# Kernel tuning notes

Hardware: AMD Instinct MI355X
Metric: run time of the kernel (lower is better)

The kernel has to match this reference:

```python
import jax, jax.numpy as jnp
import numpy as np

HIDDEN = 512

def setup_inputs() -> dict:
    key = jax.random.key(0)
    ks = jax.random.split(key, 8)
    S, Bsz, I, H, D = 512, 64, 512, HIDDEN, 2
    return {
        "X": jax.random.normal(ks[0], (S, Bsz, I), jnp.float32),
        "W": jax.random.normal(ks[1], (D, 4 * H, I), jnp.float32) * 0.05,
        "R": jax.random.normal(ks[2], (D, 4 * H, H), jnp.float32) * 0.05,
        "B": jax.random.normal(ks[3], (D, 8 * H), jnp.float32) * 0.05,
        "sequence_lens": jax.random.randint(ks[4], (Bsz,), 0, S, jnp.int32),
        "initial_h": jax.random.normal(ks[5], (D, Bsz, H), jnp.float32) * 0.1,
        "initial_c": jax.random.normal(ks[6], (D, Bsz, H), jnp.float32) * 0.1,
        "P": jax.random.normal(ks[7], (D, 3 * H), jnp.float32) * 0.05,
    }

def _run_dir(Xg, R_d, Rb_d, h0, c0, P_d, seq_lens, ts, H):
    # Gate layout along 4H axis: i, o, f, c (ONNX order used by the source).
    P_i, P_f, P_o = P_d[:H], P_d[H:2 * H], P_d[2 * H:3 * H]

    def step(carry, inp):
        h, c = carry
        xg, t = inp                              # xg: [B,4H] precomputed X@W^T + Wb
        g = xg + h @ R_d.T + Rb_d                # [B,4H]
        i_t = jax.nn.sigmoid(g[:, :H] + P_i * c)
        f_t = jax.nn.sigmoid(g[:, 2 * H:3 * H] + P_f * c)
        c_til = jnp.tanh(g[:, 3 * H:4 * H])
        c_new = f_t * c + i_t * c_til
        o_t = jax.nn.sigmoid(g[:, H:2 * H] + P_o * c_new)
        h_new = o_t * jnp.tanh(c_new)
        mask = (t < seq_lens).astype(h_new.dtype)[:, None]
        h_new = h_new * mask + h0 * (1 - mask)
        c_new = c_new * mask + c0 * (1 - mask)
        return (h_new, c_new), h_new

    (h_f, c_f), hs = jax.lax.scan(step, (h0, c0), (Xg[ts], jnp.asarray(ts)))
    return hs, h_f, c_f

def reference(X, W, R, B, sequence_lens, initial_h, initial_c, P):
    S, Bsz, I = X.shape
    D = W.shape[0]
    H = W.shape[1] // 4
    Wb = B[:, :4 * H]
    Rb = B[:, 4 * H:8 * H]
    # Batch the input projection over all timesteps once: [D,S,B,4H]
    Xg_all = jnp.einsum('sbi,dgi->dsbg', X, W) + Wb[:, None, None, :]
    Ys, Yhs, Ycs = [], [], []
    for d in range(D):
        ts = np.arange(S) if d == 0 else np.arange(S)[::-1].copy()
        hs, h_f, c_f = _run_dir(Xg_all[d], R[d], Rb[d], initial_h[d],
                                initial_c[d], P[d], sequence_lens, ts, H)
        if d == 1:
            hs = hs[::-1]                         # scan emitted reversed time order
        Ys.append(hs)
        Yhs.append(h_f)
        Ycs.append(c_f)
    Y = jnp.stack(Ys, axis=1)                     # [S, D, B, H]
    Y_h = jnp.stack(Yhs, axis=0)                  # [D, B, H]
    Y_c = jnp.stack(Ycs, axis=0)                  # [D, B, H]
    return Y, Y_h, Y_c
```

## Files before the change

### kernel.cpp

```cpp
#include <hip/hip_runtime.h>
#include <stdint.h>
#include <stddef.h>

#define S_LEN 512
#define BATCH 64
#define ISZ   512
#define HID   512
#define NDIR  2

typedef short bf16x8 __attribute__((ext_vector_type(8)));
typedef unsigned short u16x8 __attribute__((ext_vector_type(8)));
typedef float f32x4 __attribute__((ext_vector_type(4)));

#define XB_ELEMS  ((size_t)S_LEN * 4 * 8192)
#define HH_ELEMS  ((size_t)NDIR * 513 * 4 * 8192)
#define CNT_BYTES ((size_t)16416)
#define XB_BYTES  (XB_ELEMS * 2)
#define HH_BYTES  (HH_ELEMS * 2)

__device__ __forceinline__ unsigned short f2bf(float f) {
    unsigned int u = __float_as_uint(f);
    u += 0x7fffu + ((u >> 16) & 1u);
    return (unsigned short)(u >> 16);
}

__device__ __forceinline__ int l2_load_i32(const int* p) {
    int v;
    asm volatile("global_load_dword %0, %1, off sc0\n\t"
                 "s_waitcnt vmcnt(0)"
                 : "=v"(v) : "v"(p) : "memory");
    return v;
}

__global__ void k_convX(const float* __restrict__ X, unsigned short* __restrict__ Xb) {
    int gu = blockIdx.x * 256 + threadIdx.x;
    int t   = gu >> 12;
    int rem = gu & 4095;
    int b   = rem >> 6;
    int u   = rem & 63;
    const float* src = X + ((size_t)(t * 64 + b)) * 512 + u * 8;
    float4 a = *(const float4*)(src);
    float4 c = *(const float4*)(src + 4);
    u16x8 o;
    o[0]=f2bf(a.x); o[1]=f2bf(a.y); o[2]=f2bf(a.z); o[3]=f2bf(a.w);
    o[4]=f2bf(c.x); o[5]=f2bf(c.y); o[6]=f2bf(c.z); o[7]=f2bf(c.w);
    int i = b >> 4, br = b & 15;
    size_t off = ((size_t)(t * 4 + i)) * 8192 + (size_t)br * 512 + (size_t)((u ^ (b & 7)) << 3);
    *(u16x8*)(Xb + off) = o;
}

__global__ void k_initH(const float* __restrict__ h0, unsigned short* __restrict__ hh) {
    int gu = blockIdx.x * 256 + threadIdx.x;
    int d   = gu >> 12;
    int rem = gu & 4095;
    int b   = rem >> 6;
    int u   = rem & 63;
    const float* src = h0 + ((size_t)(d * 64 + b)) * 512 + u * 8;
    float4 a = *(const float4*)(src);
    float4 c = *(const float4*)(src + 4);
    u16x8 o;
    o[0]=f2bf(a.x); o[1]=f2bf(a.y); o[2]=f2bf(a.z); o[3]=f2bf(a.w);
    o[4]=f2bf(c.x); o[5]=f2bf(c.y); o[6]=f2bf(c.z); o[7]=f2bf(c.w);
    int i = b >> 4, br = b & 15;
    size_t blk = ((size_t)d * 513 + 0) * 4 + i;
    size_t off = blk * 8192 + (size_t)br * 512 + (size_t)((u ^ (b & 7)) << 3);
    *(u16x8*)(hh + off) = o;
}

__launch_bounds__(256, 1)
__global__ void k_lstm(const float* __restrict__ W, const float* __restrict__ R,
                       const float* __restrict__ Bb, const int* __restrict__ slen,
                       const float* __restrict__ h0g, const float* __restrict__ c0g,
                       const float* __restrict__ P,
                       const unsigned short* __restrict__ Xb,
                       unsigned short* __restrict__ hh,
                       int* __restrict__ cnt,
                       float* __restrict__ Y) {
    __shared__ __align__(16) float gbuf[4 * 256];
    __shared__ int s_xcd[256];
    __shared__ unsigned char s_inv[256];
    __shared__ int s_role, s_fast;

    const int tid = threadIdx.x;
    const int bx  = blockIdx.x;

    int* const arrive = cnt;
    int* const xcdtab = cnt + 288;

    if (tid == 0) {
        int x;
        asm volatile("s_getreg_b32 %0, hwreg(HW_REG_XCC_ID)" : "=s"(x));
        x &= 0xf;
        __hip_atomic_store(&xcdtab[bx], x + 1, __ATOMIC_RELAXED, __HIP_MEMORY_SCOPE_AGENT);
        asm volatile("s_waitcnt vmcnt(0)" ::: "memory");
        __hip_atomic_fetch_add(arrive, 1, __ATOMIC_RELAXED, __HIP_MEMORY_SCOPE_AGENT);
        int iters = 0;
        while (__hip_atomic_load(arrive, __ATOMIC_RELAXED, __HIP_MEMORY_SCOPE_AGENT) < 256) {
            __builtin_amdgcn_s_sleep(1);
            if (++iters > 2000000) break;
        }
    }
    __syncthreads();
    s_xcd[tid] = __hip_atomic_load(&xcdtab[tid], __ATOMIC_RELAXED, __HIP_MEMORY_SCOPE_AGENT) - 1;
    __syncthreads();
    {
        const int myx = s_xcd[tid];
        int r = 0;
        for (int b = 0; b < 256; ++b) {
            const int xb = s_xcd[b];
            r += (int)((xb < myx) | ((xb == myx) & (b < tid)));
        }
        s_inv[r] = (unsigned char)(myx & 0xff);
        if (tid == bx) s_role = r;
    }
    __syncthreads();
    if (tid == 0) {
        const int g0 = s_role & ~31;
        int uni = 1;
        for (int q = 1; q < 32; ++q) uni &= (int)(s_inv[g0 + q] == s_inv[g0]);
        int distinct = 1;
        for (int q = 1; q < 256; ++q) distinct += (int)(s_inv[q] != s_inv[q - 1]);
        s_fast = uni & (int)(distinct >= 2);
    }
    __syncthreads();
    const int  role = s_role;
    const bool fast = (s_fast != 0);
    const int  d = role >> 7;
    const int  i = (role >> 5) & 3;
    const int  j = role & 31;
    int* const gcnt = cnt + 32 + ((role >> 5) << 5);

    const int w  = tid >> 6;
    const int l  = tid & 63;
    const int lr = l & 15;
    const int lq = l >> 4;

    bf16x8 Wf[16], Rf[16];
    {
        const int row = w * 512 + j * 16 + lr;
        const float* wp = W + ((size_t)(d * 2048 + row)) * 512;
        const float* rp = R + ((size_t)(d * 2048 + row)) * 512;
#pragma unroll
        for (int kc = 0; kc < 16; ++kc) {
            int k0 = kc * 32 + lq * 8;
            float4 a = *(const float4*)(wp + k0);
            float4 b4 = *(const float4*)(wp + k0 + 4);
            bf16x8 f;
            f[0]=(short)f2bf(a.x);  f[1]=(short)f2bf(a.y);  f[2]=(short)f2bf(a.z);  f[3]=(short)f2bf(a.w);
            f[4]=(short)f2bf(b4.x); f[5]=(short)f2bf(b4.y); f[6]=(short)f2bf(b4.z); f[7]=(short)f2bf(b4.w);
            Wf[kc] = f;
            a  = *(const float4*)(rp + k0);
            b4 = *(const float4*)(rp + k0 + 4);
            bf16x8 g;
            g[0]=(short)f2bf(a.x);  g[1]=(short)f2bf(a.y);  g[2]=(short)f2bf(a.z);  g[3]=(short)f2bf(a.w);
            g[4]=(short)f2bf(b4.x); g[5]=(short)f2bf(b4.y); g[6]=(short)f2bf(b4.z); g[7]=(short)f2bf(b4.w);
            Rf[kc] = g;
        }
    }

    const int eb = tid >> 4;
    const int ec = tid & 15;
    const int bg = i * 16 + eb;
    const int kh = j * 16 + ec;
    const float bias_i = Bb[d * 4096 + 0 * 512 + kh] + Bb[d * 4096 + 2048 + 0 * 512 + kh];
    const float bias_o = Bb[d * 4096 + 1 * 512 + kh] + Bb[d * 4096 + 2048 + 1 * 512 + kh];
    const float bias_f = Bb[d * 4096 + 2 * 512 + kh] + Bb[d * 4096 + 2048 + 2 * 512 + kh];
    const float bias_c = Bb[d * 4096 + 3 * 512 + kh] + Bb[d * 4096 + 2048 + 3 * 512 + kh];
    const float Pi = P[d * 1536 + kh];
    const float Pf = P[d * 1536 + 512 + kh];
    const float Po = P[d * 1536 + 1024 + kh];
    const int   sl  = slen[bg];
    const float h0v = h0g[((size_t)d * 64 + bg) * 512 + kh];
    const float c0v = c0g[((size_t)d * 64 + bg) * 512 + kh];
    float c_state = c0v;

    const int rbase = lr * 512;
    const int swz   = lr & 7;

    const int peb = tid >> 4;
    const int cp  = (tid & 15) >> 1;
    const size_t puo = (size_t)peb * 256
                     + (size_t)((((2 * j + (cp >> 2)) ^ (peb & 7)) << 2) + (cp & 3));

    for (int ts = 0; ts < 512; ++ts) {
        const int t = (d == 0) ? ts : (511 - ts);

        f32x4 acc = {0.f, 0.f, 0.f, 0.f};
        {
            const unsigned short* xsrc = Xb + ((size_t)(t * 4 + i)) * 8192;
#pragma unroll
            for (int kc = 0; kc < 16; ++kc) {
                int u = (kc * 4 + lq) ^ swz;
                bf16x8 a = *(const bf16x8*)(xsrc + rbase + u * 8);
                acc = __builtin_amdgcn_mfma_f32_16x16x32_bf16(a, Wf[kc], acc, 0, 0, 0);
            }
        }

        if (ts > 0) {
            if (tid == 0) {
                const int target = 32 * ts;
                int iters = 0;
                if (fast) {
                    while (l2_load_i32(gcnt) < target) {
                        __builtin_amdgcn_s_sleep(1);
                        if (++iters > 4000000) break;
                    }
                } else {
                    while (__hip_atomic_load(gcnt, __ATOMIC_RELAXED,
                                             __HIP_MEMORY_SCOPE_AGENT) < target) {
                        __builtin_amdgcn_s_sleep(1);
                        if (++iters > 4000000) break;
                    }
                }
            }
            __syncthreads();
        }

        {
            const unsigned short* hsrc16 = hh + (((size_t)d * 513 + ts) * 4 + i) * 8192;
            if (fast) {
                bf16x8 hf[16];
#pragma unroll
                for (int kc = 0; kc < 16; ++kc) {
                    const int u = (kc * 4 + lq) ^ swz;
                    hf[kc] = *(const bf16x8*)(hsrc16 + rbase + u * 8);
                }
#pragma unroll
                for (int kc = 0; kc < 16; ++kc)
                    acc = __builtin_amdgcn_mfma_f32_16x16x32_bf16(hf[kc], Rf[kc], acc, 0, 0, 0);
            } else {
                const unsigned int* hsrc = (const unsigned int*)hsrc16;
                unsigned int hv[64];
#pragma unroll
                for (int kc = 0; kc < 16; ++kc) {
                    int u = (kc * 4 + lq) ^ swz;
                    const unsigned int* p = hsrc + (lr * 256 + u * 4);
                    hv[kc * 4 + 0] = __hip_atomic_load(p + 0, __ATOMIC_RELAXED, __HIP_MEMORY_SCOPE_AGENT);
                    hv[kc * 4 + 1] = __hip_atomic_load(p + 1, __ATOMIC_RELAXED, __HIP_MEMORY_SCOPE_AGENT);
                    hv[kc * 4 + 2] = __hip_atomic_load(p + 2, __ATOMIC_RELAXED, __HIP_MEMORY_SCOPE_AGENT);
                    hv[kc * 4 + 3] = __hip_atomic_load(p + 3, __ATOMIC_RELAXED, __HIP_MEMORY_SCOPE_AGENT);
                }
#pragma unroll
                for (int kc = 0; kc < 16; ++kc) {
                    union { unsigned int u[4]; bf16x8 v; } cvt;
                    cvt.u[0] = hv[kc * 4 + 0];
                    cvt.u[1] = hv[kc * 4 + 1];
                    cvt.u[2] = hv[kc * 4 + 2];
                    cvt.u[3] = hv[kc * 4 + 3];
                    acc = __builtin_amdgcn_mfma_f32_16x16x32_bf16(cvt.v, Rf[kc], acc, 0, 0, 0);
                }
            }
        }

#pragma unroll
        for (int r = 0; r < 4; ++r) {
            int b = lq * 4 + r;
            gbuf[w * 256 + b * 16 + lr] = acc[r];
        }
        __syncthreads();

        float hn, cn;
        {
            float gi = gbuf[0 * 256 + tid] + bias_i;
            float go = gbuf[1 * 256 + tid] + bias_o;
            float gf = gbuf[2 * 256 + tid] + bias_f;
            float gc = gbuf[3 * 256 + tid] + bias_c;
            float c  = c_state;
            float it = 1.f / (1.f + __expf(-(gi + Pi * c)));
            float ft = 1.f / (1.f + __expf(-(gf + Pf * c)));
            float ct = 1.f - 2.f / (__expf(2.f * gc) + 1.f);
            cn = ft * c + it * ct;
            float ot = 1.f / (1.f + __expf(-(go + Po * cn)));
            hn = ot * (1.f - 2.f / (__expf(2.f * cn) + 1.f));
            if (t >= sl) { hn = h0v; cn = c0v; }
            c_state = cn;

            Y[(((size_t)t * 2 + d) * 64 + bg) * 512 + kh] = hn;
            if (ts == 511) {
                Y[(size_t)33554432 + ((size_t)d * 64 + bg) * 512 + kh] = hn;
                Y[(size_t)33619968 + ((size_t)d * 64 + bg) * 512 + kh] = cn;
            }
        }

        {
            const unsigned int hb = (unsigned int)f2bf(hn);
            const unsigned int other = (unsigned int)__shfl_xor((int)hb, 1);
            if ((tid & 1) == 0) {
                const unsigned int v = hb | (other << 16);
                unsigned int* hdst =
                    (unsigned int*)(hh + (((size_t)d * 513 + (ts + 1)) * 4 + i) * 8192);
                if (fast) hdst[puo] = v;
                else __hip_atomic_store(hdst + puo, v, __ATOMIC_RELAXED,
                                        __HIP_MEMORY_SCOPE_AGENT);
            }
        }
        asm volatile("s_waitcnt vmcnt(0)" ::: "memory");
        __syncthreads();
        if (tid == 0) {
            if (fast) __hip_atomic_fetch_add(gcnt, 1, __ATOMIC_RELAXED,
                                             __HIP_MEMORY_SCOPE_WORKGROUP);
            else      __hip_atomic_fetch_add(gcnt, 1, __ATOMIC_RELAXED,
                                             __HIP_MEMORY_SCOPE_AGENT);
        }
    }
}

extern "C" void kernel_launch(void* const* d_in, const int* in_sizes, int n_in,
                              void* d_out, int out_size, void* d_ws, size_t ws_size,
                              hipStream_t stream) {
    const float* X  = (const float*)d_in[0];
    const float* W  = (const float*)d_in[1];
    const float* R  = (const float*)d_in[2];
    const float* Bb = (const float*)d_in[3];
    const int*   sl = (const int*)d_in[4];
    const float* h0 = (const float*)d_in[5];
    const float* c0 = (const float*)d_in[6];
    const float* P  = (const float*)d_in[7];
    float* Y = (float*)d_out;

    unsigned short* Xb  = (unsigned short*)d_ws;
    unsigned short* hh  = (unsigned short*)((char*)d_ws + XB_BYTES);
    int*            cnt = (int*)((char*)d_ws + XB_BYTES + HH_BYTES);

    hipMemsetAsync(cnt, 0, CNT_BYTES, stream);

    k_convX<<<8192, 256, 0, stream>>>(X, Xb);
    k_initH<<<32, 256, 0, stream>>>(h0, hh);
    k_lstm<<<256, 256, 0, stream>>>(W, R, Bb, sl, h0, c0, P, Xb, hh, cnt, Y);
}
```

Measured before the change: 3.837 ms.

## Replace shared arrival counter with per-block flags polled by a wavefront

```diff
diff --git a/kernel.cpp b/kernel.cpp
--- a/kernel.cpp
+++ b/kernel.cpp
@@ -24,11 +24,18 @@
     return (unsigned short)(u >> 16);
 }
 
-__device__ __forceinline__ int l2_load_i32(const int* p) {
+__device__ __forceinline__ int poll1_l2(const int* p) {
     int v;
     asm volatile("global_load_dword %0, %1, off sc0\n\t"
                  "s_waitcnt vmcnt(0)"
-                 : "=v"(v) : "v"(p) : "memory");
+                 : "=&v"(v) : "v"(p) : "memory");
+    return v;
+}
+__device__ __forceinline__ int poll1_llc(const int* p) {
+    int v;
+    asm volatile("global_load_dword %0, %1, off sc0 sc1\n\t"
+                 "s_waitcnt vmcnt(0)"
+                 : "=&v"(v) : "v"(p) : "memory");
     return v;
 }
 
@@ -77,6 +84,7 @@
                        int* __restrict__ cnt,
                        float* __restrict__ Y) {
     __shared__ __align__(16) float gbuf[4 * 256];
+    __shared__ __align__(4) unsigned short hexch[256];
     __shared__ int s_xcd[256];
     __shared__ unsigned char s_inv[256];
     __shared__ int s_role, s_fast;
@@ -128,7 +136,7 @@
     const int  d = role >> 7;
     const int  i = (role >> 5) & 3;
     const int  j = role & 31;
-    int* const gcnt = cnt + 32 + ((role >> 5) << 5);
+    int* const gflags = cnt + 576 + ((role >> 5) << 5);
 
     const int w  = tid >> 6;
     const int l  = tid & 63;
@@ -177,10 +185,13 @@
     const int rbase = lr * 512;
     const int swz   = lr & 7;
 
-    const int peb = tid >> 4;
-    const int cp  = (tid & 15) >> 1;
+    const int peb = tid >> 3;
+    const int pm  = tid & 7;
     const size_t puo = (size_t)peb * 256
-                     + (size_t)((((2 * j + (cp >> 2)) ^ (peb & 7)) << 2) + (cp & 3));
+                     + (size_t)((((2 * j + (pm >> 2)) ^ (peb & 7)) << 2) + (pm & 3));
+
+    int* const myflag = gflags + j;
+    const int* const pollp = gflags + (l & 31);
 
     for (int ts = 0; ts < 512; ++ts) {
         const int t = (d == 0) ? ts : (511 - ts);
@@ -197,17 +208,19 @@
         }
 
         if (ts > 0) {
-            if (tid == 0) {
-                const int target = 32 * ts;
+            if (w == 0) {
                 int iters = 0;
                 if (fast) {
-                    while (l2_load_i32(gcnt) < target) {
+                    for (;;) {
+                        int v = poll1_l2(pollp);
+                        if (__all(v >= ts)) break;
                         __builtin_amdgcn_s_sleep(1);
                         if (++iters > 4000000) break;
                     }
                 } else {
-                    while (__hip_atomic_load(gcnt, __ATOMIC_RELAXED,
-                                             __HIP_MEMORY_SCOPE_AGENT) < target) {
+                    for (;;) {
+                        int v = poll1_llc(pollp);
+                        if (__all(v >= ts)) break;
                         __builtin_amdgcn_s_sleep(1);
                         if (++iters > 4000000) break;
                     }
@@ -280,27 +293,25 @@
                 Y[(size_t)33554432 + ((size_t)d * 64 + bg) * 512 + kh] = hn;
                 Y[(size_t)33619968 + ((size_t)d * 64 + bg) * 512 + kh] = cn;
             }
-        }
-
-        {
-            const unsigned int hb = (unsigned int)f2bf(hn);
-            const unsigned int other = (unsigned int)__shfl_xor((int)hb, 1);
-            if ((tid & 1) == 0) {
-                const unsigned int v = hb | (other << 16);
-                unsigned int* hdst =
-                    (unsigned int*)(hh + (((size_t)d * 513 + (ts + 1)) * 4 + i) * 8192);
-                if (fast) hdst[puo] = v;
-                else __hip_atomic_store(hdst + puo, v, __ATOMIC_RELAXED,
-                                        __HIP_MEMORY_SCOPE_AGENT);
-            }
+            hexch[tid] = f2bf(hn);
+        }
+        __syncthreads();
+
+        if (tid < 128) {
+            unsigned int v = ((const unsigned int*)hexch)[tid];
+            unsigned int* hdst =
+                (unsigned int*)(hh + (((size_t)d * 513 + (ts + 1)) * 4 + i) * 8192);
+            if (fast) hdst[puo] = v;
+            else __hip_atomic_store(hdst + puo, v, __ATOMIC_RELAXED,
+                                    __HIP_MEMORY_SCOPE_AGENT);
         }
         asm volatile("s_waitcnt vmcnt(0)" ::: "memory");
         __syncthreads();
         if (tid == 0) {
-            if (fast) __hip_atomic_fetch_add(gcnt, 1, __ATOMIC_RELAXED,
-                                             __HIP_MEMORY_SCOPE_WORKGROUP);
-            else      __hip_atomic_fetch_add(gcnt, 1, __ATOMIC_RELAXED,
-                                             __HIP_MEMORY_SCOPE_AGENT);
+            if (fast) __hip_atomic_store(myflag, ts + 1, __ATOMIC_RELAXED,
+                                         __HIP_MEMORY_SCOPE_WORKGROUP);
+            else      __hip_atomic_store(myflag, ts + 1, __ATOMIC_RELAXED,
+                                         __HIP_MEMORY_SCOPE_AGENT);
         }
     }
 }
```

Result: no change. 3.765 ms (-1.9%).
